# Kernel optimization log

Hardware: AMD Instinct MI355X
Metric: run time of the kernel (lower is better)

The kernel has to match this reference:

```python
import jax, jax.numpy as jnp
import numpy as np

N = 100000      # num nodes
E = 1600000     # num edges
D_IN = 128
D_OUT = 64
PRELU_INIT = 0.25


def setup_inputs() -> dict:
    key = jax.random.key(0)
    k1, k2, k3, k4, k5 = jax.random.split(key, 5)
    node_x = jax.random.normal(k1, (N, D_IN), dtype=jnp.float32)
    edge_rows = jax.random.randint(k2, (E,), 0, N, dtype=jnp.int32)
    edge_cols = jax.random.randint(k3, (E,), 0, N, dtype=jnp.int32)
    edge_vals = jax.random.uniform(k4, (E,), dtype=jnp.float32)
    # Xavier-uniform init for weights
    limit = float(np.sqrt(6.0 / (D_IN + D_OUT)))
    weights = jax.random.uniform(k5, (D_IN, D_OUT), dtype=jnp.float32,
                                 minval=-limit, maxval=limit)
    prelu_a = jnp.float32(PRELU_INIT)
    return {"node_x": node_x, "edge_rows": edge_rows, "edge_cols": edge_cols,
            "edge_vals": edge_vals, "weights": weights, "prelu_a": prelu_a}


def reference(node_x, edge_rows, edge_cols, edge_vals, weights, prelu_a):
    # Dense projection: [N, D_IN] @ [D_IN, D_OUT] -> [N, D_OUT]
    support = jnp.matmul(node_x, weights)
    # Sparse-dense matmul: output[r] = sum_{(r,c,v) in adj} v * support[c]
    messages = edge_vals[:, None] * support[edge_cols]  # [E, D_OUT]
    output = jax.ops.segment_sum(messages, edge_rows, num_segments=N)
    # PReLU with single learned scalar
    out = jnp.where(output > 0, output, prelu_a * output)
    return (out, support)
```

## Files before the change

### kernel.cpp

```cpp
#include <hip/hip_runtime.h>

#define N_NODES 100000
#define N_EDGES 1600000
#define D_IN    128
#define D_OUT   64

#define XT_STRIDE 260
#define NBUCKETS 1563
#define NBW 782
#define G 392
#define SLICE 4096
#define M_FLAT (NBUCKETS * G)
#define SCANA_BLOCKS 599
#define GEMM_BLOCKS 391
#define CAP 2048
typedef unsigned long long ull;
typedef unsigned int uint;

__global__ __launch_bounds__(256) void k_gemm_cnt(
    const float* __restrict__ x,
    const float* __restrict__ w,
    float* __restrict__ support,
    const int* __restrict__ rows,
    uint* __restrict__ S)
{
    __shared__ float wl[D_IN * D_OUT];
    __shared__ float xT[32 * XT_STRIDE];

    const int t = threadIdx.x;

    if (blockIdx.x >= GEMM_BLOCKS) {
        uint* hist = (uint*)wl;
        const int bid = blockIdx.x - GEMM_BLOCKS;
        const int b = (bid & 7) * 49 + (bid >> 3);
        for (int i = t; i < NBW; i += 256) hist[i] = 0u;
        __syncthreads();

        const int base = b * SLICE;
#pragma unroll 4
        for (int s2 = 0; s2 < 16; ++s2) {
            const int e = base + s2 * 256 + t;
            if (e < N_EDGES) {
                const uint bk = (uint)rows[e] >> 6;
                atomicAdd(&hist[bk >> 1], 1u << ((bk & 1) * 16));
            }
        }
        __syncthreads();

        for (int i = t; i < NBUCKETS; i += 256)
            S[(size_t)i * G + b] = (hist[i >> 1] >> ((i & 1) * 16)) & 0xffffu;
        return;
    }

    const int tx = t & 7;
    const int ty = t >> 3;
    const long row0 = (long)blockIdx.x * 256;

    {
        const float4* wf  = (const float4*)w;
        float4*       wlf = (float4*)wl;
#pragma unroll
        for (int j = 0; j < 8; ++j)
            wlf[t + 256 * j] = wf[t + 256 * j];
    }

    float acc[8][8];
#pragma unroll
    for (int i = 0; i < 8; ++i)
#pragma unroll
        for (int j = 0; j < 8; ++j)
            acc[i][j] = 0.f;

    for (int kc = 0; kc < 4; ++kc) {
        const int k0 = kc * 32;
        __syncthreads();

        const int kk = tx * 4;
#pragma unroll
        for (int it = 0; it < 8; ++it) {
            const int  rg   = it * 32 + ty;
            const long grow = row0 + rg;
            float4 v = make_float4(0.f, 0.f, 0.f, 0.f);
            if (grow < N_NODES)
                v = *(const float4*)&x[grow * D_IN + k0 + kk];
            xT[(kk + 0) * XT_STRIDE + rg] = v.x;
            xT[(kk + 1) * XT_STRIDE + rg] = v.y;
            xT[(kk + 2) * XT_STRIDE + rg] = v.z;
            xT[(kk + 3) * XT_STRIDE + rg] = v.w;
        }
        __syncthreads();

#pragma unroll 8
        for (int k = 0; k < 32; ++k) {
            const float4 a0 = *(const float4*)&xT[k * XT_STRIDE + ty * 8];
            const float4 a1 = *(const float4*)&xT[k * XT_STRIDE + ty * 8 + 4];
            const float4 b0 = *(const float4*)&wl[(k0 + k) * D_OUT + tx * 8];
            const float4 b1 = *(const float4*)&wl[(k0 + k) * D_OUT + tx * 8 + 4];
            const float av[8] = {a0.x, a0.y, a0.z, a0.w, a1.x, a1.y, a1.z, a1.w};
            const float bv[8] = {b0.x, b0.y, b0.z, b0.w, b1.x, b1.y, b1.z, b1.w};
#pragma unroll
            for (int i = 0; i < 8; ++i)
#pragma unroll
                for (int j = 0; j < 8; ++j)
                    acc[i][j] = fmaf(av[i], bv[j], acc[i][j]);
        }
    }

#pragma unroll
    for (int i = 0; i < 8; ++i) {
        const long r = row0 + ty * 8 + i;
        if (r < N_NODES) {
            float4 o0 = make_float4(acc[i][0], acc[i][1], acc[i][2], acc[i][3]);
            float4 o1 = make_float4(acc[i][4], acc[i][5], acc[i][6], acc[i][7]);
            *(float4*)&support[r * D_OUT + tx * 8]     = o0;
            *(float4*)&support[r * D_OUT + tx * 8 + 4] = o1;
        }
    }
}

__global__ __launch_bounds__(256) void k_scanA(
    uint* __restrict__ S, uint* __restrict__ bsum)
{
    __shared__ uint s[256];
    const int t = threadIdx.x;
    const size_t base = (size_t)blockIdx.x * 1024 + (size_t)t * 4;
    uint4 v = make_uint4(0u, 0u, 0u, 0u);
    if (base < M_FLAT) v = *(const uint4*)&S[base];
    const uint tsum = v.x + v.y + v.z + v.w;
    s[t] = tsum;
    __syncthreads();
#pragma unroll
    for (int off = 1; off < 256; off <<= 1) {
        const uint add = (t >= off) ? s[t - off] : 0u;
        __syncthreads();
        s[t] += add;
        __syncthreads();
    }
    const uint eb = s[t] - tsum;
    if (t == 255) bsum[blockIdx.x] = s[255];
    if (base < M_FLAT) {
        uint4 o;
        o.x = eb; o.y = eb + v.x; o.z = o.y + v.y; o.w = o.z + v.z;
        *(uint4*)&S[base] = o;
    }
}

__global__ __launch_bounds__(1024) void k_scanB(uint* __restrict__ bsum)
{
    __shared__ uint s[1024];
    const int t = threadIdx.x;
    const uint v = (t < SCANA_BLOCKS) ? bsum[t] : 0u;
    s[t] = v;
    __syncthreads();
#pragma unroll
    for (int off = 1; off < 1024; off <<= 1) {
        const uint add = (t >= off) ? s[t - off] : 0u;
        __syncthreads();
        s[t] += add;
        __syncthreads();
    }
    if (t < SCANA_BLOCKS) bsum[t] = s[t] - v;
}

__global__ __launch_bounds__(256) void k_scatter(
    const int* __restrict__ rows, const int* __restrict__ cols,
    const float* __restrict__ vals, const uint* __restrict__ S,
    const uint* __restrict__ bsum, ull* __restrict__ pairs)
{
    __shared__ uint cur[NBUCKETS];
    __shared__ uint bs[SCANA_BLOCKS + 1];
    const int t = threadIdx.x;
    const int b = (blockIdx.x & 7) * 49 + (blockIdx.x >> 3);

    for (int i = t; i < SCANA_BLOCKS; i += 256) bs[i] = bsum[i];
    __syncthreads();
    for (int i = t; i < NBUCKETS; i += 256) {
        const size_t f = (size_t)i * G + b;
        cur[i] = S[f] + bs[f >> 10];
    }
    __syncthreads();

    const int base = b * SLICE;
#pragma unroll 4
    for (int s2 = 0; s2 < 16; ++s2) {
        const int e = base + s2 * 256 + t;
        if (e < N_EDGES) {
            const uint r  = (uint)rows[e];
            const uint bk = r >> 6;
            const uint rl = r & 63u;
            const uint pos = atomicAdd(&cur[bk], 1u);
            pairs[pos] = ((ull)__float_as_uint(vals[e]) << 32)
                       | (rl << 17) | (uint)cols[e];
        }
    }
}

__global__ __launch_bounds__(256) void k_bucket(
    const uint* __restrict__ S, const uint* __restrict__ bsum,
    const ull* __restrict__ pairs, const float* __restrict__ support,
    const float* __restrict__ prelu_a, float* __restrict__ out)
{
    __shared__ ull srt[CAP];
    __shared__ uint h[64], ex[64], rowoff[64], cur[64];
    const int k = blockIdx.x;
    const int t = threadIdx.x, w = t >> 6, lane = t & 63;

    const size_t f0 = (size_t)k * G;
    const int beg = (int)(S[f0] + bsum[f0 >> 10]);
    int end;
    if (k == NBUCKETS - 1) end = N_EDGES;
    else {
        const size_t f1 = f0 + G;
        end = (int)(S[f1] + bsum[f1 >> 10]);
    }
    const int n = end - beg;
    const float a = prelu_a[0];

    if (t < 64) h[t] = 0u;
    __syncthreads();

    if (n <= CAP) {
        for (int i = t; i < n; i += 256)
            atomicAdd(&h[((uint)pairs[beg + i] >> 17) & 63u], 1u);
        __syncthreads();

        if (t < 64) ex[t] = h[t];
        __syncthreads();
#pragma unroll
        for (int off = 1; off < 64; off <<= 1) {
            const uint add = (t >= off && t < 64) ? ex[t - off] : 0u;
            __syncthreads();
            if (t < 64) ex[t] += add;
            __syncthreads();
        }
        if (t < 64) {
            rowoff[t] = ex[t] - h[t];
            cur[t]    = rowoff[t];
        }
        __syncthreads();

        for (int i = t; i < n; i += 256) {
            const ull p = pairs[beg + i];
            const uint pos = atomicAdd(&cur[((uint)p >> 17) & 63u], 1u);
            srt[pos] = p;
        }
        __syncthreads();

        for (int q = 0; q < 16; ++q) {
            const int rl  = w * 16 + q;
            const long row = (long)k * 64 + rl;
            if (row >= N_NODES) break;
            const int st  = (int)rowoff[rl];
            const int deg = (int)h[rl];

            float acc = 0.f;
            int j = 0;
            for (; j + 8 <= deg; j += 8) {
                ull p[8];
#pragma unroll
                for (int u = 0; u < 8; ++u) p[u] = srt[st + j + u];
                float sv[8];
#pragma unroll
                for (int u = 0; u < 8; ++u)
                    sv[u] = support[(size_t)((uint)p[u] & 0x1ffffu) * D_OUT + lane];
#pragma unroll
                for (int u = 0; u < 8; ++u)
                    acc = fmaf(__uint_as_float((uint)(p[u] >> 32)), sv[u], acc);
            }
            for (; j + 4 <= deg; j += 4) {
                ull p[4];
#pragma unroll
                for (int u = 0; u < 4; ++u) p[u] = srt[st + j + u];
                float sv[4];
#pragma unroll
                for (int u = 0; u < 4; ++u)
                    sv[u] = support[(size_t)((uint)p[u] & 0x1ffffu) * D_OUT + lane];
#pragma unroll
                for (int u = 0; u < 4; ++u)
                    acc = fmaf(__uint_as_float((uint)(p[u] >> 32)), sv[u], acc);
            }
            for (; j < deg; ++j) {
                const ull p = srt[st + j];
                acc = fmaf(__uint_as_float((uint)(p >> 32)),
                           support[(size_t)((uint)p & 0x1ffffu) * D_OUT + lane], acc);
            }
            out[row * D_OUT + lane] = acc > 0.f ? acc : a * acc;
        }
    } else {
        for (int q = 0; q < 16; ++q) {
            const int rl  = w * 16 + q;
            const long row = (long)k * 64 + rl;
            if (row >= N_NODES) break;
            float acc = 0.f;
            for (int i = 0; i < n; ++i) {
                const ull p = pairs[beg + i];
                if ((((uint)p >> 17) & 63u) == (uint)rl)
                    acc = fmaf(__uint_as_float((uint)(p >> 32)),
                               support[(size_t)((uint)p & 0x1ffffu) * D_OUT + lane],
                               acc);
            }
            out[row * D_OUT + lane] = acc > 0.f ? acc : a * acc;
        }
    }
}

extern "C" void kernel_launch(void* const* d_in, const int* in_sizes, int n_in,
                              void* d_out, int out_size, void* d_ws, size_t ws_size,
                              hipStream_t stream) {
    const float* x    = (const float*)d_in[0];
    const int*   rows = (const int*)d_in[1];
    const int*   cols = (const int*)d_in[2];
    const float* vals = (const float*)d_in[3];
    const float* w    = (const float*)d_in[4];
    const float* pa   = (const float*)d_in[5];

    float* out     = (float*)d_out;
    float* support = out + (size_t)N_NODES * D_OUT;

    uint* S     = (uint*)d_ws;
    uint* bsum  = S + (size_t)SCANA_BLOCKS * 1024;
    ull*  pairs = (ull*)(bsum + 1024);

    k_gemm_cnt<<<GEMM_BLOCKS + G, 256, 0, stream>>>(x, w, support, rows, S);
    k_scanA   <<<SCANA_BLOCKS, 256, 0, stream>>>(S, bsum);
    k_scanB   <<<1, 1024, 0, stream>>>(bsum);
    k_scatter <<<G, 256, 0, stream>>>(rows, cols, vals, S, bsum, pairs);
    k_bucket  <<<NBUCKETS, 256, 0, stream>>>(S, bsum, pairs, support, pa, out);
}
```

Before: 242.9 us.

## Fold block-sum scan into scatter kernel and vectorize edge loads

Removes the single-block scanB launch by having every scatter block redundantly scan the 599 block sums in shared memory, with block 0 writing the result to a separate buffer that the bucket kernel reads. The histogram and scatter loops now load rows, cols and vals as int4/float4, four edges per thread. This saves one kernel launch and its serial dependency. In exchange each scatter block does extra scan work and sync rounds, and the scatter write order within buckets changes.

```diff
diff --git a/kernel.cpp b/kernel.cpp
--- a/kernel.cpp
+++ b/kernel.cpp
@@ -37,12 +37,15 @@
         __syncthreads();
 
         const int base = b * SLICE;
-#pragma unroll 4
-        for (int s2 = 0; s2 < 16; ++s2) {
-            const int e = base + s2 * 256 + t;
+#pragma unroll
+        for (int s2 = 0; s2 < 4; ++s2) {
+            const int e = base + s2 * 1024 + t * 4;
             if (e < N_EDGES) {
-                const uint bk = (uint)rows[e] >> 6;
-                atomicAdd(&hist[bk >> 1], 1u << ((bk & 1) * 16));
+                const int4 r4 = *(const int4*)&rows[e];
+                atomicAdd(&hist[(uint)r4.x >> 7], 1u << ((((uint)r4.x >> 6) & 1) * 16));
+                atomicAdd(&hist[(uint)r4.y >> 7], 1u << ((((uint)r4.y >> 6) & 1) * 16));
+                atomicAdd(&hist[(uint)r4.z >> 7], 1u << ((((uint)r4.z >> 6) & 1) * 16));
+                atomicAdd(&hist[(uint)r4.w >> 7], 1u << ((((uint)r4.w >> 6) & 1) * 16));
             }
         }
         __syncthreads();
@@ -145,35 +148,42 @@
     }
 }
 
-__global__ __launch_bounds__(1024) void k_scanB(uint* __restrict__ bsum)
-{
-    __shared__ uint s[1024];
-    const int t = threadIdx.x;
-    const uint v = (t < SCANA_BLOCKS) ? bsum[t] : 0u;
-    s[t] = v;
-    __syncthreads();
-#pragma unroll
-    for (int off = 1; off < 1024; off <<= 1) {
-        const uint add = (t >= off) ? s[t - off] : 0u;
-        __syncthreads();
-        s[t] += add;
-        __syncthreads();
-    }
-    if (t < SCANA_BLOCKS) bsum[t] = s[t] - v;
-}
-
 __global__ __launch_bounds__(256) void k_scatter(
     const int* __restrict__ rows, const int* __restrict__ cols,
     const float* __restrict__ vals, const uint* __restrict__ S,
-    const uint* __restrict__ bsum, ull* __restrict__ pairs)
+    const uint* __restrict__ bsum, uint* __restrict__ bsum2,
+    ull* __restrict__ pairs)
 {
     __shared__ uint cur[NBUCKETS];
-    __shared__ uint bs[SCANA_BLOCKS + 1];
+    __shared__ uint bs[SCANA_BLOCKS];
+    __shared__ uint meta[256];
     const int t = threadIdx.x;
-    const int b = (blockIdx.x & 7) * 49 + (blockIdx.x >> 3);
+    const int bid = blockIdx.x;
+    const int b = (bid & 7) * 49 + (bid >> 3);
 
     for (int i = t; i < SCANA_BLOCKS; i += 256) bs[i] = bsum[i];
     __syncthreads();
+
+    uint carry = 0;
+    for (int c0 = 0; c0 < SCANA_BLOCKS; c0 += 256) {
+        const int i = c0 + t;
+        const uint v = (i < SCANA_BLOCKS) ? bs[i] : 0u;
+        meta[t] = v;
+        __syncthreads();
+#pragma unroll
+        for (int off = 1; off < 256; off <<= 1) {
+            const uint add = (t >= off) ? meta[t - off] : 0u;
+            __syncthreads();
+            meta[t] += add;
+            __syncthreads();
+        }
+        if (i < SCANA_BLOCKS) bs[i] = carry + meta[t] - v;
+        carry += meta[255];
+        __syncthreads();
+    }
+    if (bid == 0)
+        for (int i = t; i < SCANA_BLOCKS; i += 256) bsum2[i] = bs[i];
+
     for (int i = t; i < NBUCKETS; i += 256) {
         const size_t f = (size_t)i * G + b;
         cur[i] = S[f] + bs[f >> 10];
@@ -181,22 +191,43 @@
     __syncthreads();
 
     const int base = b * SLICE;
-#pragma unroll 4
-    for (int s2 = 0; s2 < 16; ++s2) {
-        const int e = base + s2 * 256 + t;
+#pragma unroll
+    for (int s2 = 0; s2 < 4; ++s2) {
+        const int e = base + s2 * 1024 + t * 4;
         if (e < N_EDGES) {
-            const uint r  = (uint)rows[e];
-            const uint bk = r >> 6;
-            const uint rl = r & 63u;
-            const uint pos = atomicAdd(&cur[bk], 1u);
-            pairs[pos] = ((ull)__float_as_uint(vals[e]) << 32)
-                       | (rl << 17) | (uint)cols[e];
+            const int4   r4 = *(const int4*)&rows[e];
+            const int4   c4 = *(const int4*)&cols[e];
+            const float4 v4 = *(const float4*)&vals[e];
+            {
+                const uint r = (uint)r4.x;
+                const uint pos = atomicAdd(&cur[r >> 6], 1u);
+                pairs[pos] = ((ull)__float_as_uint(v4.x) << 32)
+                           | ((r & 63u) << 17) | (uint)c4.x;
+            }
+            {
+                const uint r = (uint)r4.y;
+                const uint pos = atomicAdd(&cur[r >> 6], 1u);
+                pairs[pos] = ((ull)__float_as_uint(v4.y) << 32)
+                           | ((r & 63u) << 17) | (uint)c4.y;
+            }
+            {
+                const uint r = (uint)r4.z;
+                const uint pos = atomicAdd(&cur[r >> 6], 1u);
+                pairs[pos] = ((ull)__float_as_uint(v4.z) << 32)
+                           | ((r & 63u) << 17) | (uint)c4.z;
+            }
+            {
+                const uint r = (uint)r4.w;
+                const uint pos = atomicAdd(&cur[r >> 6], 1u);
+                pairs[pos] = ((ull)__float_as_uint(v4.w) << 32)
+                           | ((r & 63u) << 17) | (uint)c4.w;
+            }
         }
     }
 }
 
 __global__ __launch_bounds__(256) void k_bucket(
-    const uint* __restrict__ S, const uint* __restrict__ bsum,
+    const uint* __restrict__ S, const uint* __restrict__ bsum2,
     const ull* __restrict__ pairs, const float* __restrict__ support,
     const float* __restrict__ prelu_a, float* __restrict__ out)
 {
@@ -206,12 +237,12 @@
     const int t = threadIdx.x, w = t >> 6, lane = t & 63;
 
     const size_t f0 = (size_t)k * G;
-    const int beg = (int)(S[f0] + bsum[f0 >> 10]);
+    const int beg = (int)(S[f0] + bsum2[f0 >> 10]);
     int end;
     if (k == NBUCKETS - 1) end = N_EDGES;
     else {
         const size_t f1 = f0 + G;
-        end = (int)(S[f1] + bsum[f1 >> 10]);
+        end = (int)(S[f1] + bsum2[f1 >> 10]);
     }
     const int n = end - beg;
     const float a = prelu_a[0];
@@ -319,11 +350,11 @@
 
     uint* S     = (uint*)d_ws;
     uint* bsum  = S + (size_t)SCANA_BLOCKS * 1024;
-    ull*  pairs = (ull*)(bsum + 1024);
+    uint* bsum2 = bsum + 1024;
+    ull*  pairs = (ull*)(bsum2 + 1024);
 
     k_gemm_cnt<<<GEMM_BLOCKS + G, 256, 0, stream>>>(x, w, support, rows, S);
     k_scanA   <<<SCANA_BLOCKS, 256, 0, stream>>>(S, bsum);
-    k_scanB   <<<1, 1024, 0, stream>>>(bsum);
-    k_scatter <<<G, 256, 0, stream>>>(rows, cols, vals, S, bsum, pairs);
-    k_bucket  <<<NBUCKETS, 256, 0, stream>>>(S, bsum, pairs, support, pa, out);
-}
+    k_scatter <<<G, 256, 0, stream>>>(rows, cols, vals, S, bsum, bsum2, pairs);
+    k_bucket  <<<NBUCKETS, 256, 0, stream>>>(S, bsum2, pairs, support, pa, out);
+}
```

Measured after the change: 229.2 us. 1.06x faster.
